# Optimization experiments

Measured on AMD Instinct MI355X. Metric: run time of the kernel, lower is better.

The kernel has to match this reference:

```python
import jax, jax.numpy as jnp
import numpy as np

N = 100000
E = 1600000
F_IN = 128
HID = 128
C = 10
NEG_SLOPE = 0.2


def setup_inputs() -> dict:
    key = jax.random.key(0)
    ks = jax.random.split(key, 12)
    x = jax.random.normal(ks[0], (N, F_IN), dtype=jnp.float32)
    edge_index = jax.random.randint(ks[1], (2, E), 0, N, dtype=jnp.int64)
    batch = jnp.zeros((N,), dtype=jnp.int64)
    s1 = 1.0 / np.sqrt(F_IN)
    s2 = 1.0 / np.sqrt(HID)
    return {
        "x": x,
        "edge_index": edge_index,
        "batch": batch,
        "W1": jax.random.normal(ks[2], (F_IN, HID), dtype=jnp.float32) * s1,
        "a_src1": jax.random.normal(ks[3], (HID,), dtype=jnp.float32) * s2,
        "a_dst1": jax.random.normal(ks[4], (HID,), dtype=jnp.float32) * s2,
        "b1": jnp.zeros((HID,), dtype=jnp.float32),
        "W2": jax.random.normal(ks[5], (HID, HID), dtype=jnp.float32) * s2,
        "a_src2": jax.random.normal(ks[6], (HID,), dtype=jnp.float32) * s2,
        "a_dst2": jax.random.normal(ks[7], (HID,), dtype=jnp.float32) * s2,
        "b2": jnp.zeros((HID,), dtype=jnp.float32),
        "Wlin": jax.random.normal(ks[8], (HID, C), dtype=jnp.float32) * s2,
        "blin": jnp.zeros((C,), dtype=jnp.float32),
    }


def gat_conv(x, src, dst, W, a_src, a_dst, b):
    # PyG GATConv, heads=1: h = xW; alpha_e = softmax_dst(leaky_relu(a_src.h[src] + a_dst.h[dst]))
    h = x @ W                                  # [N, H]
    alpha_s = h @ a_src                        # [N]
    alpha_d = h @ a_dst                        # [N]
    e = jax.nn.leaky_relu(alpha_s[src] + alpha_d[dst], NEG_SLOPE)  # [E]
    m = jax.ops.segment_max(e, dst, num_segments=N)                # per-dst max (stable softmax)
    ex = jnp.exp(e - m[dst])
    denom = jax.ops.segment_sum(ex, dst, num_segments=N)
    alpha = ex / (denom[dst] + 1e-16)          # [E]
    out = jax.ops.segment_sum(h[src] * alpha[:, None], dst, num_segments=N)
    return out + b


def reference(x, edge_index, batch, W1, a_src1, a_dst1, b1, W2, a_src2, a_dst2, b2, Wlin, blin):
    x = x.astype(jnp.float32)
    loops = jnp.arange(N, dtype=edge_index.dtype)
    src = jnp.concatenate([edge_index[0], loops])  # add_self_loops=True
    dst = jnp.concatenate([edge_index[1], loops])
    h = jax.nn.relu(gat_conv(x, src, dst, W1, a_src1, a_dst1, b1))
    h = jax.nn.relu(gat_conv(h, src, dst, W2, a_src2, a_dst2, b2))
    # dropout(p=0.5) is identity in eval mode
    return h @ Wlin + blin
```

## Files before the change

kernel.cpp:

```cpp
#include <hip/hip_runtime.h>

#define N_NODES 100000
#define N_EDGES 1600000
#define TOTE    (N_EDGES + N_NODES)
#define NEG     0.2f
#define NB      ((N_NODES + 255) >> 8)
#define BCAP    5120

typedef __attribute__((ext_vector_type(8))) short bf16x8;
typedef __attribute__((ext_vector_type(4))) float floatx4;

__device__ __forceinline__ unsigned short f2bf(float f) {
  unsigned int u = __float_as_uint(f);
  u += 0x7fffu + ((u >> 16) & 1u);
  return (unsigned short)(u >> 16);
}
__device__ __forceinline__ float bf_lo(unsigned int r) { return __uint_as_float(r << 16); }
__device__ __forceinline__ float bf_hi(unsigned int r) { return __uint_as_float(r & 0xffff0000u); }

__global__ __launch_bounds__(256) void k_wprep(const float* __restrict__ W1, const float* __restrict__ W2,
                                               unsigned short* __restrict__ B1hi, unsigned short* __restrict__ B1lo,
                                               unsigned short* __restrict__ B2hi, unsigned short* __restrict__ B2lo,
                                               int* __restrict__ bucketCnt) {
  int b = blockIdx.x;
  int t = threadIdx.x;
  if (b == 16) {
    for (int i = t; i < NB * 16; i += 256) bucketCnt[i] = 0;
    return;
  }
  const float* W = (b < 8) ? W1 : W2;
  unsigned short* Bh = (b < 8) ? B1hi : B2hi;
  unsigned short* Bl = (b < 8) ? B1lo : B2lo;
  int ntile = b & 7;
  int kq = t >> 6, lane = t & 63;
  int q = lane >> 4, m = lane & 15;
  int n = ntile * 16 + m;
  union { unsigned short us[8]; uint4 u4; } hi, lo;
#pragma unroll
  for (int j = 0; j < 8; ++j) {
    int k = kq * 32 + q * 8 + j;
    float w = W[(size_t)k * 128 + n];
    unsigned int u = __float_as_uint(w);
    hi.us[j] = (unsigned short)(u >> 16);
    float res = w - __uint_as_float(u & 0xffff0000u);
    lo.us[j] = f2bf(res);
  }
  size_t fo = ((size_t)(ntile * 4 + kq) * 64 + lane) * 8;
  *reinterpret_cast<uint4*>(Bh + fo) = hi.u4;
  *reinterpret_cast<uint4*>(Bl + fo) = lo.u4;
}

__global__ __launch_bounds__(256) void k_binA(const int* __restrict__ ei, int* __restrict__ bucketCnt,
                                              unsigned int* __restrict__ binned) {
  __shared__ int hist[NB];
  __shared__ int cur[NB];
  int t = threadIdx.x;
  for (int b = t; b < NB; b += 256) hist[b] = 0;
  __syncthreads();
  unsigned int pk[16]; int bk[16];
#pragma unroll
  for (int j = 0; j < 16; ++j) {
    int idx = blockIdx.x * 4096 + j * 256 + t;
    if (idx < N_EDGES) {
      int s = ei[idx], d = ei[N_EDGES + idx];
      bk[j] = d >> 8;
      pk[j] = ((unsigned int)s << 8) | (unsigned int)(d & 255);
      atomicAdd(&hist[bk[j]], 1);
    } else bk[j] = -1;
  }
  __syncthreads();
  for (int b = t; b < NB; b += 256) {
    int h = hist[b];
    if (h) cur[b] = b * BCAP + atomicAdd(&bucketCnt[b * 16], h);
  }
  __syncthreads();
#pragma unroll
  for (int j = 0; j < 16; ++j) {
    if (bk[j] >= 0) {
      int pos = atomicAdd(&cur[bk[j]], 1);
      binned[pos] = pk[j];
    }
  }
}

__global__ __launch_bounds__(512) void k_bin_scan(const int* __restrict__ bucketCnt,
                                                  int* __restrict__ binOffs) {
  __shared__ int sc[512];
  int t = threadIdx.x;
  int v = (t < NB) ? bucketCnt[t * 16] : 0;
  sc[t] = v; __syncthreads();
  for (int off = 1; off < 512; off <<= 1) {
    int x = (t >= off) ? sc[t - off] : 0;
    __syncthreads();
    sc[t] += x;
    __syncthreads();
  }
  int excl = sc[t] - v;
  if (t <= NB) binOffs[t] = excl;
}

__global__ __launch_bounds__(256) void k_binB(const unsigned int* __restrict__ binned,
                                              const int* __restrict__ binOffs,
                                              int* __restrict__ offs, int* __restrict__ srcs) {
  __shared__ int cnt[256];
  __shared__ int sc[256];
  __shared__ int cur[256];
  int b = blockIdx.x;
  int t = threadIdx.x;
  int node0 = b << 8;
  int nNodes = min(256, N_NODES - node0);
  int cntE = binOffs[b + 1] - binOffs[b];
  int e0 = b * BCAP, e1 = e0 + cntE;
  int base = binOffs[b] + node0;

  cnt[t] = 0; __syncthreads();
  for (int i = e0 + t; i < e1; i += 256) atomicAdd(&cnt[binned[i] & 255u], 1);
  __syncthreads();

  int v = (t < nNodes) ? cnt[t] + 1 : 0;
  sc[t] = v; __syncthreads();
  for (int off = 1; off < 256; off <<= 1) {
    int x = (t >= off) ? sc[t - off] : 0;
    __syncthreads();
    sc[t] += x;
    __syncthreads();
  }
  int excl = sc[t] - v;
  if (t < nNodes) {
    offs[node0 + t] = base + excl;
    srcs[base + excl] = node0 + t;
  }
  cur[t] = excl + 1;
  __syncthreads();

  for (int i = e0 + t; i < e1; i += 256) {
    unsigned int e = binned[i];
    int j = (int)(e & 255u);
    int s = (int)(e >> 8);
    int p = atomicAdd(&cur[j], 1);
    srcs[base + p] = s;
  }
  if (b == 0 && t == 0) offs[N_NODES] = TOTE;
}

template <bool SPLIT>
__global__ __launch_bounds__(256) void k_gemm_mfma(const void* __restrict__ Aptr,
                                                   const unsigned short* __restrict__ Bhi,
                                                   const unsigned short* __restrict__ Blo,
                                                   unsigned short* __restrict__ Cb,
                                                   const float* __restrict__ avS, const float* __restrict__ avD,
                                                   float* __restrict__ aS, float* __restrict__ aD,
                                                   float* __restrict__ slotS, float* __restrict__ slotD) {
  __shared__ unsigned short sC[64 * 136];
  __shared__ float redS[64 * 4], redD[64 * 4];
  __shared__ float mS[64], mD[64];
  int t = threadIdx.x;
  int w = t >> 6, lane = t & 63;
  int q = lane >> 4, m = lane & 15;
  int rbase = blockIdx.x * 64;

  floatx4 acc[4][2];
#pragma unroll
  for (int mt = 0; mt < 4; ++mt)
#pragma unroll
    for (int nt = 0; nt < 2; ++nt) acc[mt][nt] = (floatx4){0.f, 0.f, 0.f, 0.f};

#pragma unroll
  for (int k0 = 0; k0 < 4; ++k0) {
    bf16x8 Bh[2], Bl[2], Ah[4], Al[4];
#pragma unroll
    for (int nt = 0; nt < 2; ++nt) {
      int ntg = w * 2 + nt;
      size_t fo = ((size_t)(ntg * 4 + k0) * 64 + lane) * 8;
      Bh[nt] = *reinterpret_cast<const bf16x8*>(Bhi + fo);
      Bl[nt] = *reinterpret_cast<const bf16x8*>(Blo + fo);
    }
#pragma unroll
    for (int mt = 0; mt < 4; ++mt) {
      int row = rbase + mt * 16 + m;
      row = min(row, N_NODES - 1);
      if constexpr (SPLIT) {
        const float* ap = (const float*)Aptr + (size_t)row * 128 + k0 * 32 + q * 8;
        float4 v0 = *reinterpret_cast<const float4*>(ap);
        float4 v1 = *reinterpret_cast<const float4*>(ap + 4);
        float av[8] = {v0.x, v0.y, v0.z, v0.w, v1.x, v1.y, v1.z, v1.w};
        union { unsigned short us[8]; bf16x8 v; } uh, ul;
#pragma unroll
        for (int j = 0; j < 8; ++j) {
          unsigned int u = __float_as_uint(av[j]);
          uh.us[j] = (unsigned short)(u >> 16);
          float res = av[j] - __uint_as_float(u & 0xffff0000u);
          ul.us[j] = f2bf(res);
        }
        Ah[mt] = uh.v; Al[mt] = ul.v;
      } else {
        const unsigned short* ap = (const unsigned short*)Aptr + (size_t)row * 128 + k0 * 32 + q * 8;
        Ah[mt] = *reinterpret_cast<const bf16x8*>(ap);
      }
    }
#pragma unroll
    for (int mt = 0; mt < 4; ++mt)
#pragma unroll
      for (int nt = 0; nt < 2; ++nt) {
        acc[mt][nt] = __builtin_amdgcn_mfma_f32_16x16x32_bf16(Ah[mt], Bh[nt], acc[mt][nt], 0, 0, 0);
        acc[mt][nt] = __builtin_amdgcn_mfma_f32_16x16x32_bf16(Ah[mt], Bl[nt], acc[mt][nt], 0, 0, 0);
        if constexpr (SPLIT)
          acc[mt][nt] = __builtin_amdgcn_mfma_f32_16x16x32_bf16(Al[mt], Bh[nt], acc[mt][nt], 0, 0, 0);
      }
  }

  float avs[2], avd[2];
#pragma unroll
  for (int nt = 0; nt < 2; ++nt) {
    int c = w * 32 + nt * 16 + m;
    avs[nt] = avS[c];
    avd[nt] = avD[c];
  }
#pragma unroll
  for (int mt = 0; mt < 4; ++mt)
#pragma unroll
    for (int r = 0; r < 4; ++r) {
      float ps = acc[mt][0][r] * avs[0] + acc[mt][1][r] * avs[1];
      float pd = acc[mt][0][r] * avd[0] + acc[mt][1][r] * avd[1];
      ps += __shfl_xor(ps, 1); pd += __shfl_xor(pd, 1);
      ps += __shfl_xor(ps, 2); pd += __shfl_xor(pd, 2);
      ps += __shfl_xor(ps, 4); pd += __shfl_xor(pd, 4);
      ps += __shfl_xor(ps, 8); pd += __shfl_xor(pd, 8);
      if (m == 0) {
        int rl = mt * 16 + q * 4 + r;
        redS[rl * 4 + w] = ps;
        redD[rl * 4 + w] = pd;
      }
    }

#pragma unroll
  for (int mt = 0; mt < 4; ++mt)
#pragma unroll
    for (int nt = 0; nt < 2; ++nt)
#pragma unroll
      for (int r = 0; r < 4; ++r) {
        int rl = mt * 16 + q * 4 + r;
        int cl = w * 32 + nt * 16 + m;
        sC[rl * 136 + cl] = f2bf(acc[mt][nt][r]);
      }
  __syncthreads();

#pragma unroll
  for (int i = 0; i < 4; ++i) {
    int idx = i * 256 + t;
    int rl = idx >> 4, kk = idx & 15;
    int gr = rbase + rl;
    if (gr < N_NODES)
      *reinterpret_cast<uint4*>(Cb + (size_t)gr * 128 + kk * 8) =
          *reinterpret_cast<const uint4*>(sC + rl * 136 + kk * 8);
  }

  if (t < 64) {
    int gr = rbase + t;
    bool ok = gr < N_NODES;
    float ps = redS[t * 4] + redS[t * 4 + 1] + redS[t * 4 + 2] + redS[t * 4 + 3];
    float pd = redD[t * 4] + redD[t * 4 + 1] + redD[t * 4 + 2] + redD[t * 4 + 3];
    if (ok) { aS[gr] = ps; aD[gr] = pd; }
    mS[t] = ok ? ps : -1e30f;
    mD[t] = ok ? pd : -1e30f;
  }
  __syncthreads();
#pragma unroll
  for (int off = 32; off > 0; off >>= 1) {
    if (t < off) { mS[t] = fmaxf(mS[t], mS[t + off]); mD[t] = fmaxf(mD[t], mD[t + off]); }
    __syncthreads();
  }
  if (t == 0) { slotS[blockIdx.x] = mS[0]; slotD[blockIdx.x] = mD[0]; }
}

__global__ __launch_bounds__(256) void k_gmax(const float* __restrict__ slotS,
                                              const float* __restrict__ slotD,
                                              int n, float* __restrict__ gMh) {
  __shared__ float sS[256], sD[256];
  int t = threadIdx.x;
  float ms = -1e30f, md = -1e30f;
  for (int i = t; i < n; i += 256) { ms = fmaxf(ms, slotS[i]); md = fmaxf(md, slotD[i]); }
  sS[t] = ms; sD[t] = md;
  __syncthreads();
#pragma unroll
  for (int off = 128; off > 0; off >>= 1) {
    if (t < off) { sS[t] = fmaxf(sS[t], sS[t + off]); sD[t] = fmaxf(sD[t], sD[t + off]); }
    __syncthreads();
  }
  if (t == 0) {
    float M = sS[0] + sD[0];
    gMh[0] = (M > 0.f) ? M : NEG * M;
  }
}

#define FMA8(E, R)                                     \
  do {                                                 \
    acc[0] += (E) * bf_lo((R).x); acc[1] += (E) * bf_hi((R).x); \
    acc[2] += (E) * bf_lo((R).y); acc[3] += (E) * bf_hi((R).y); \
    acc[4] += (E) * bf_lo((R).z); acc[5] += (E) * bf_hi((R).z); \
    acc[6] += (E) * bf_lo((R).w); acc[7] += (E) * bf_hi((R).w); \
  } while (0)

__global__ __launch_bounds__(256) void k_aggregate(const unsigned short* __restrict__ hb,
                                                   const float* __restrict__ aS,
                                                   const float* __restrict__ aD,
                                                   const int* __restrict__ offs,
                                                   const int* __restrict__ srcs,
                                                   const float* __restrict__ bias,
                                                   const float* __restrict__ gMh,
                                                   unsigned short* __restrict__ outb) {
  __shared__ float2 pairs[16 * 17];
  int t = threadIdx.x;
  int g = t >> 4;
  int l = t & 15;
  int dst = blockIdx.x * 16 + g;
  float Mh = gMh[0];
  int beg = offs[dst], end = offs[dst + 1];
  float adn = aD[dst];
  float denom = 0.f;
  float acc[8];
#pragma unroll
  for (int k = 0; k < 8; ++k) acc[k] = 0.f;
  const int pbase = g * 17;

  for (int chunk = beg; chunk < end; chunk += 16) {
    int i = chunk + l;
    float ex = 0.f; int s = 0;
    if (i < end) {
      s = srcs[i];
      float e = aS[s] + adn;
      e = (e > 0.f) ? e : NEG * e;
      ex = __expf(e - Mh);
    }
    denom += ex;
    pairs[pbase + l] = make_float2(ex, __int_as_float(s));
    int cnt = min(16, end - chunk);
    int j = 0;
    for (; j + 4 <= cnt; j += 4) {
      float2 p0 = pairs[pbase + j + 0];
      float2 p1 = pairs[pbase + j + 1];
      float2 p2 = pairs[pbase + j + 2];
      float2 p3 = pairs[pbase + j + 3];
      uint4 r0 = *reinterpret_cast<const uint4*>(hb + (size_t)__float_as_int(p0.y) * 128 + l * 8);
      uint4 r1 = *reinterpret_cast<const uint4*>(hb + (size_t)__float_as_int(p1.y) * 128 + l * 8);
      uint4 r2 = *reinterpret_cast<const uint4*>(hb + (size_t)__float_as_int(p2.y) * 128 + l * 8);
      uint4 r3 = *reinterpret_cast<const uint4*>(hb + (size_t)__float_as_int(p3.y) * 128 + l * 8);
      FMA8(p0.x, r0);
      FMA8(p1.x, r1);
      FMA8(p2.x, r2);
      FMA8(p3.x, r3);
    }
    for (; j < cnt; ++j) {
      float2 pp = pairs[pbase + j];
      uint4 r = *reinterpret_cast<const uint4*>(hb + (size_t)__float_as_int(pp.y) * 128 + l * 8);
      FMA8(pp.x, r);
    }
  }
  denom += __shfl_xor(denom, 1);
  denom += __shfl_xor(denom, 2);
  denom += __shfl_xor(denom, 4);
  denom += __shfl_xor(denom, 8);
  float inv = 1.f / (denom + 1e-16f);
  float4 b0 = *reinterpret_cast<const float4*>(bias + l * 8);
  float4 b1 = *reinterpret_cast<const float4*>(bias + l * 8 + 4);
  float o0 = fmaxf(acc[0] * inv + b0.x, 0.f), o1 = fmaxf(acc[1] * inv + b0.y, 0.f);
  float o2 = fmaxf(acc[2] * inv + b0.z, 0.f), o3 = fmaxf(acc[3] * inv + b0.w, 0.f);
  float o4 = fmaxf(acc[4] * inv + b1.x, 0.f), o5 = fmaxf(acc[5] * inv + b1.y, 0.f);
  float o6 = fmaxf(acc[6] * inv + b1.z, 0.f), o7 = fmaxf(acc[7] * inv + b1.w, 0.f);
  union { unsigned short us[8]; uint4 u4; } oo;
  oo.us[0] = f2bf(o0); oo.us[1] = f2bf(o1); oo.us[2] = f2bf(o2); oo.us[3] = f2bf(o3);
  oo.us[4] = f2bf(o4); oo.us[5] = f2bf(o5); oo.us[6] = f2bf(o6); oo.us[7] = f2bf(o7);
  *reinterpret_cast<uint4*>(outb + (size_t)dst * 128 + l * 8) = oo.u4;
}

#define UNPK(V, B)                                     \
  do {                                                 \
    h[(B)+0] = bf_lo((V).x); h[(B)+1] = bf_hi((V).x);  \
    h[(B)+2] = bf_lo((V).y); h[(B)+3] = bf_hi((V).y);  \
    h[(B)+4] = bf_lo((V).z); h[(B)+5] = bf_hi((V).z);  \
    h[(B)+6] = bf_lo((V).w); h[(B)+7] = bf_hi((V).w);  \
  } while (0)

__global__ __launch_bounds__(256) void k_linear(const unsigned short* __restrict__ hb,
                                                const float* __restrict__ Wl,
                                                const float* __restrict__ bl,
                                                float* __restrict__ out) {
  __shared__ float sWt[10 * 144];
  __shared__ float sbl[10];
  int t = threadIdx.x;
  if (t < 128) {
    int jj = t >> 5, ii = t & 31;
#pragma unroll
    for (int c = 0; c < 10; ++c) sWt[c * 144 + jj * 36 + ii] = Wl[t * 10 + c];
  }
  if (t < 10) sbl[t] = bl[t];
  __syncthreads();
  int node = blockIdx.x * 64 + (t >> 2);
  int j = t & 3;
  if (node >= N_NODES) return;
  const unsigned short* hrow = hb + (size_t)node * 128 + j * 32;
  uint4 v0 = *reinterpret_cast<const uint4*>(hrow);
  uint4 v1 = *reinterpret_cast<const uint4*>(hrow + 8);
  uint4 v2 = *reinterpret_cast<const uint4*>(hrow + 16);
  uint4 v3 = *reinterpret_cast<const uint4*>(hrow + 24);
  float h[32];
  UNPK(v0, 0); UNPK(v1, 8); UNPK(v2, 16); UNPK(v3, 24);
  float p[10];
#pragma unroll
  for (int c = 0; c < 10; ++c) {
    const float4* wp = reinterpret_cast<const float4*>(&sWt[c * 144 + j * 36]);
    float s = 0.f;
#pragma unroll
    for (int qq = 0; qq < 8; ++qq) {
      float4 wv = wp[qq];
      s += h[qq * 4 + 0] * wv.x + h[qq * 4 + 1] * wv.y + h[qq * 4 + 2] * wv.z + h[qq * 4 + 3] * wv.w;
    }
    p[c] = s;
  }
#pragma unroll
  for (int c = 0; c < 10; ++c) {
    p[c] += __shfl_xor(p[c], 1);
    p[c] += __shfl_xor(p[c], 2);
  }
  if (j == 0) {
    float* orow = out + (size_t)node * 10;
    *reinterpret_cast<float2*>(orow + 0) = make_float2(p[0] + sbl[0], p[1] + sbl[1]);
    *reinterpret_cast<float2*>(orow + 2) = make_float2(p[2] + sbl[2], p[3] + sbl[3]);
    *reinterpret_cast<float2*>(orow + 4) = make_float2(p[4] + sbl[4], p[5] + sbl[5]);
    *reinterpret_cast<float2*>(orow + 6) = make_float2(p[6] + sbl[6], p[7] + sbl[7]);
    *reinterpret_cast<float2*>(orow + 8) = make_float2(p[8] + sbl[8], p[9] + sbl[9]);
  }
}

extern "C" void kernel_launch(void* const* d_in, const int* in_sizes, int n_in,
                              void* d_out, int out_size, void* d_ws, size_t ws_size,
                              hipStream_t stream) {
  const float* x   = (const float*)d_in[0];
  const int*   ei  = (const int*)d_in[1];
  const float* W1  = (const float*)d_in[3];
  const float* as1 = (const float*)d_in[4];
  const float* ad1 = (const float*)d_in[5];
  const float* b1  = (const float*)d_in[6];
  const float* W2  = (const float*)d_in[7];
  const float* as2 = (const float*)d_in[8];
  const float* ad2 = (const float*)d_in[9];
  const float* b2  = (const float*)d_in[10];
  const float* Wl  = (const float*)d_in[11];
  const float* bl  = (const float*)d_in[12];
  float* out = (float*)d_out;

  char* p = (char*)d_ws;
  unsigned short* hb   = (unsigned short*)p; p += (size_t)N_NODES * 128 * sizeof(unsigned short);
  unsigned short* hagg = (unsigned short*)p; p += (size_t)N_NODES * 128 * sizeof(unsigned short);
  float* aS    = (float*)p; p += (size_t)N_NODES * sizeof(float);
  float* aD    = (float*)p; p += (size_t)N_NODES * sizeof(float);
  int* offs    = (int*)p;   p += (size_t)(N_NODES + 4) * sizeof(int);
  int* srcs    = (int*)p;   p += (size_t)TOTE * sizeof(int);
  int* bucketCnt = (int*)p; p += (size_t)NB * 16 * sizeof(int);
  int* binOffs   = (int*)p; p += (size_t)(NB + 4) * sizeof(int);
  float* slotS = (float*)p; p += 2048 * sizeof(float);
  float* slotD = (float*)p; p += 2048 * sizeof(float);
  float* gMh = (float*)p;   p += 4 * sizeof(float);
  unsigned short* B1hi = (unsigned short*)p; p += 128 * 128 * sizeof(unsigned short);
  unsigned short* B1lo = (unsigned short*)p; p += 128 * 128 * sizeof(unsigned short);
  unsigned short* B2hi = (unsigned short*)p; p += 128 * 128 * sizeof(unsigned short);
  unsigned short* B2lo = (unsigned short*)p; p += 128 * 128 * sizeof(unsigned short);
  unsigned int* binned = (unsigned int*)hagg;

  int binBlocks = (N_EDGES + 4095) / 4096;

  k_wprep<<<17, 256, 0, stream>>>(W1, W2, B1hi, B1lo, B2hi, B2lo, bucketCnt);
  k_binA<<<binBlocks, 256, 0, stream>>>(ei, bucketCnt, binned);
  k_bin_scan<<<1, 512, 0, stream>>>(bucketCnt, binOffs);
  k_binB<<<NB, 256, 0, stream>>>(binned, binOffs, offs, srcs);

  int gemmBlocks = (N_NODES + 63) / 64;
  int aggBlocks  = N_NODES / 16;
  int linBlocks  = (N_NODES + 63) / 64;

  k_gemm_mfma<true><<<gemmBlocks, 256, 0, stream>>>(x, B1hi, B1lo, hb, as1, ad1, aS, aD, slotS, slotD);
  k_gmax<<<1, 256, 0, stream>>>(slotS, slotD, gemmBlocks, gMh);
  k_aggregate<<<aggBlocks, 256, 0, stream>>>(hb, aS, aD, offs, srcs, b1, gMh, hagg);
  k_gemm_mfma<false><<<gemmBlocks, 256, 0, stream>>>(hagg, B2hi, B2lo, hb, as2, ad2, aS, aD, slotS, slotD);
  k_gmax<<<1, 256, 0, stream>>>(slotS, slotD, gemmBlocks, gMh);
  k_aggregate<<<aggBlocks, 256, 0, stream>>>(hb, aS, aD, offs, srcs, b2, gMh, hagg);
  k_linear<<<linBlocks, 256, 0, stream>>>(hagg, Wl, bl, out);
}
```

Baseline: 365.3 us.

## Use one wavefront per destination with register-pipelined gathers; fuse final linear into aggregation

The aggregation kernel now assigns a full 64-lane wavefront to each destination node, with four 16-lane subgroups each handling a strided share of the edges. Edge weights and source indices are broadcast with shuffles instead of shared memory, and eight row gathers are kept in flight in registers. Partial sums are then reduced across subgroups. The second-layer aggregation also applies the final 128x10 linear layer directly, which removes the separate linear kernel and the round trip of the hidden features through memory. In exchange it uses more shuffles and more registers, and wastes lanes on low-degree nodes; it also shifts work per block from 16 to 4 destinations.

```diff
diff --git a/kernel.cpp b/kernel.cpp
--- a/kernel.cpp
+++ b/kernel.cpp
@@ -301,6 +301,7 @@
     acc[6] += (E) * bf_lo((R).w); acc[7] += (E) * bf_hi((R).w); \
   } while (0)
 
+template <bool FINAL>
 __global__ __launch_bounds__(256) void k_aggregate(const unsigned short* __restrict__ hb,
                                                    const float* __restrict__ aS,
                                                    const float* __restrict__ aD,
@@ -308,12 +309,27 @@
                                                    const int* __restrict__ srcs,
                                                    const float* __restrict__ bias,
                                                    const float* __restrict__ gMh,
-                                                   unsigned short* __restrict__ outb) {
-  __shared__ float2 pairs[16 * 17];
-  int t = threadIdx.x;
-  int g = t >> 4;
-  int l = t & 15;
-  int dst = blockIdx.x * 16 + g;
+                                                   unsigned short* __restrict__ outb,
+                                                   const float* __restrict__ Wl,
+                                                   const float* __restrict__ bl,
+                                                   float* __restrict__ out) {
+  __shared__ float sWt[10 * 144];
+  __shared__ float sbl[10];
+  int t = threadIdx.x;
+  if constexpr (FINAL) {
+    if (t < 128) {
+      int jj = t >> 5, ii = t & 31;
+#pragma unroll
+      for (int c = 0; c < 10; ++c) sWt[c * 144 + jj * 36 + ii] = Wl[t * 10 + c];
+    }
+    if (t < 10) sbl[t] = bl[t];
+    __syncthreads();
+  }
+  int w = t >> 6;
+  int tl = t & 63;
+  int sub = tl >> 4;
+  int l = tl & 15;
+  int dst = blockIdx.x * 4 + w;
   float Mh = gMh[0];
   int beg = offs[dst], end = offs[dst + 1];
   float adn = aD[dst];
@@ -321,114 +337,115 @@
   float acc[8];
 #pragma unroll
   for (int k = 0; k < 8; ++k) acc[k] = 0.f;
-  const int pbase = g * 17;
-
-  for (int chunk = beg; chunk < end; chunk += 16) {
-    int i = chunk + l;
-    float ex = 0.f; int s = 0;
+  const unsigned short* hbl = hb + l * 8;
+
+  uint4 r0, r1, r2, r3, r4, r5, r6, r7;
+
+  for (int base = beg; base < end; base += 64) {
+    int i = base + tl;
+    int sx = 0; float ex = 0.f;
     if (i < end) {
-      s = srcs[i];
-      float e = aS[s] + adn;
+      sx = srcs[i];
+      float e = aS[sx] + adn;
       e = (e > 0.f) ? e : NEG * e;
       ex = __expf(e - Mh);
     }
     denom += ex;
-    pairs[pbase + l] = make_float2(ex, __int_as_float(s));
-    int cnt = min(16, end - chunk);
-    int j = 0;
-    for (; j + 4 <= cnt; j += 4) {
-      float2 p0 = pairs[pbase + j + 0];
-      float2 p1 = pairs[pbase + j + 1];
-      float2 p2 = pairs[pbase + j + 2];
-      float2 p3 = pairs[pbase + j + 3];
-      uint4 r0 = *reinterpret_cast<const uint4*>(hb + (size_t)__float_as_int(p0.y) * 128 + l * 8);
-      uint4 r1 = *reinterpret_cast<const uint4*>(hb + (size_t)__float_as_int(p1.y) * 128 + l * 8);
-      uint4 r2 = *reinterpret_cast<const uint4*>(hb + (size_t)__float_as_int(p2.y) * 128 + l * 8);
-      uint4 r3 = *reinterpret_cast<const uint4*>(hb + (size_t)__float_as_int(p3.y) * 128 + l * 8);
-      FMA8(p0.x, r0);
-      FMA8(p1.x, r1);
-      FMA8(p2.x, r2);
-      FMA8(p3.x, r3);
-    }
-    for (; j < cnt; ++j) {
-      float2 pp = pairs[pbase + j];
-      uint4 r = *reinterpret_cast<const uint4*>(hb + (size_t)__float_as_int(pp.y) * 128 + l * 8);
-      FMA8(pp.x, r);
-    }
-  }
+    int cnt = end - base; if (cnt > 64) cnt = 64;
+
+#define BS(P) __shfl(sx, 4 * (P) + sub, 64)
+#define BE(P) __shfl(ex, 4 * (P) + sub, 64)
+#define ISS(R, P)                                                                   \
+    do {                                                                            \
+      if (4 * (P) < cnt) {                                                          \
+        int s_ = BS(P);                                                             \
+        R = *reinterpret_cast<const uint4*>(hbl + ((size_t)(unsigned)s_ << 7));     \
+      }                                                                             \
+    } while (0)
+#define STP(R, P)                       \
+    do {                                \
+      float e_ = BE(P);                 \
+      FMA8(e_, R);                      \
+      ISS(R, (P) + 8);                  \
+    } while (0)
+
+    ISS(r0, 0); ISS(r1, 1); ISS(r2, 2); ISS(r3, 3);
+    ISS(r4, 4); ISS(r5, 5); ISS(r6, 6); ISS(r7, 7);
+    do {
+      STP(r0, 0);  if (cnt <= 4)  break;
+      STP(r1, 1);  if (cnt <= 8)  break;
+      STP(r2, 2);  if (cnt <= 12) break;
+      STP(r3, 3);  if (cnt <= 16) break;
+      STP(r4, 4);  if (cnt <= 20) break;
+      STP(r5, 5);  if (cnt <= 24) break;
+      STP(r6, 6);  if (cnt <= 28) break;
+      STP(r7, 7);  if (cnt <= 32) break;
+      STP(r0, 8);  if (cnt <= 36) break;
+      STP(r1, 9);  if (cnt <= 40) break;
+      STP(r2, 10); if (cnt <= 44) break;
+      STP(r3, 11); if (cnt <= 48) break;
+      STP(r4, 12); if (cnt <= 52) break;
+      STP(r5, 13); if (cnt <= 56) break;
+      STP(r6, 14); if (cnt <= 60) break;
+      STP(r7, 15);
+    } while (0);
+#undef BS
+#undef BE
+#undef ISS
+#undef STP
+  }
+
   denom += __shfl_xor(denom, 1);
   denom += __shfl_xor(denom, 2);
   denom += __shfl_xor(denom, 4);
   denom += __shfl_xor(denom, 8);
+  denom += __shfl_xor(denom, 16);
+  denom += __shfl_xor(denom, 32);
   float inv = 1.f / (denom + 1e-16f);
+#pragma unroll
+  for (int k = 0; k < 8; ++k) {
+    acc[k] += __shfl_xor(acc[k], 16);
+    acc[k] += __shfl_xor(acc[k], 32);
+  }
+
   float4 b0 = *reinterpret_cast<const float4*>(bias + l * 8);
   float4 b1 = *reinterpret_cast<const float4*>(bias + l * 8 + 4);
   float o0 = fmaxf(acc[0] * inv + b0.x, 0.f), o1 = fmaxf(acc[1] * inv + b0.y, 0.f);
   float o2 = fmaxf(acc[2] * inv + b0.z, 0.f), o3 = fmaxf(acc[3] * inv + b0.w, 0.f);
   float o4 = fmaxf(acc[4] * inv + b1.x, 0.f), o5 = fmaxf(acc[5] * inv + b1.y, 0.f);
   float o6 = fmaxf(acc[6] * inv + b1.z, 0.f), o7 = fmaxf(acc[7] * inv + b1.w, 0.f);
-  union { unsigned short us[8]; uint4 u4; } oo;
-  oo.us[0] = f2bf(o0); oo.us[1] = f2bf(o1); oo.us[2] = f2bf(o2); oo.us[3] = f2bf(o3);
-  oo.us[4] = f2bf(o4); oo.us[5] = f2bf(o5); oo.us[6] = f2bf(o6); oo.us[7] = f2bf(o7);
-  *reinterpret_cast<uint4*>(outb + (size_t)dst * 128 + l * 8) = oo.u4;
-}
-
-#define UNPK(V, B)                                     \
-  do {                                                 \
-    h[(B)+0] = bf_lo((V).x); h[(B)+1] = bf_hi((V).x);  \
-    h[(B)+2] = bf_lo((V).y); h[(B)+3] = bf_hi((V).y);  \
-    h[(B)+4] = bf_lo((V).z); h[(B)+5] = bf_hi((V).z);  \
-    h[(B)+6] = bf_lo((V).w); h[(B)+7] = bf_hi((V).w);  \
-  } while (0)
-
-__global__ __launch_bounds__(256) void k_linear(const unsigned short* __restrict__ hb,
-                                                const float* __restrict__ Wl,
-                                                const float* __restrict__ bl,
-                                                float* __restrict__ out) {
-  __shared__ float sWt[10 * 144];
-  __shared__ float sbl[10];
-  int t = threadIdx.x;
-  if (t < 128) {
-    int jj = t >> 5, ii = t & 31;
-#pragma unroll
-    for (int c = 0; c < 10; ++c) sWt[c * 144 + jj * 36 + ii] = Wl[t * 10 + c];
-  }
-  if (t < 10) sbl[t] = bl[t];
-  __syncthreads();
-  int node = blockIdx.x * 64 + (t >> 2);
-  int j = t & 3;
-  if (node >= N_NODES) return;
-  const unsigned short* hrow = hb + (size_t)node * 128 + j * 32;
-  uint4 v0 = *reinterpret_cast<const uint4*>(hrow);
-  uint4 v1 = *reinterpret_cast<const uint4*>(hrow + 8);
-  uint4 v2 = *reinterpret_cast<const uint4*>(hrow + 16);
-  uint4 v3 = *reinterpret_cast<const uint4*>(hrow + 24);
-  float h[32];
-  UNPK(v0, 0); UNPK(v1, 8); UNPK(v2, 16); UNPK(v3, 24);
-  float p[10];
-#pragma unroll
-  for (int c = 0; c < 10; ++c) {
-    const float4* wp = reinterpret_cast<const float4*>(&sWt[c * 144 + j * 36]);
-    float s = 0.f;
-#pragma unroll
-    for (int qq = 0; qq < 8; ++qq) {
-      float4 wv = wp[qq];
-      s += h[qq * 4 + 0] * wv.x + h[qq * 4 + 1] * wv.y + h[qq * 4 + 2] * wv.z + h[qq * 4 + 3] * wv.w;
-    }
-    p[c] = s;
-  }
-#pragma unroll
-  for (int c = 0; c < 10; ++c) {
-    p[c] += __shfl_xor(p[c], 1);
-    p[c] += __shfl_xor(p[c], 2);
-  }
-  if (j == 0) {
-    float* orow = out + (size_t)node * 10;
-    *reinterpret_cast<float2*>(orow + 0) = make_float2(p[0] + sbl[0], p[1] + sbl[1]);
-    *reinterpret_cast<float2*>(orow + 2) = make_float2(p[2] + sbl[2], p[3] + sbl[3]);
-    *reinterpret_cast<float2*>(orow + 4) = make_float2(p[4] + sbl[4], p[5] + sbl[5]);
-    *reinterpret_cast<float2*>(orow + 6) = make_float2(p[6] + sbl[6], p[7] + sbl[7]);
-    *reinterpret_cast<float2*>(orow + 8) = make_float2(p[8] + sbl[8], p[9] + sbl[9]);
+
+  if constexpr (!FINAL) {
+    if (sub == 0) {
+      union { unsigned short us[8]; uint4 u4; } oo;
+      oo.us[0] = f2bf(o0); oo.us[1] = f2bf(o1); oo.us[2] = f2bf(o2); oo.us[3] = f2bf(o3);
+      oo.us[4] = f2bf(o4); oo.us[5] = f2bf(o5); oo.us[6] = f2bf(o6); oo.us[7] = f2bf(o7);
+      *reinterpret_cast<uint4*>(outb + (size_t)dst * 128 + l * 8) = oo.u4;
+    }
+  } else {
+    float p[10];
+#pragma unroll
+    for (int c = 0; c < 10; ++c) {
+      const float4* wp = reinterpret_cast<const float4*>(&sWt[c * 144 + (l >> 2) * 36 + (l & 3) * 8]);
+      float4 w0 = wp[0], w1 = wp[1];
+      p[c] = o0 * w0.x + o1 * w0.y + o2 * w0.z + o3 * w0.w +
+             o4 * w1.x + o5 * w1.y + o6 * w1.z + o7 * w1.w;
+    }
+#pragma unroll
+    for (int c = 0; c < 10; ++c) {
+      p[c] += __shfl_xor(p[c], 1);
+      p[c] += __shfl_xor(p[c], 2);
+      p[c] += __shfl_xor(p[c], 4);
+      p[c] += __shfl_xor(p[c], 8);
+    }
+    if (tl == 0) {
+      float* orow = out + (size_t)dst * 10;
+      *reinterpret_cast<float2*>(orow + 0) = make_float2(p[0] + sbl[0], p[1] + sbl[1]);
+      *reinterpret_cast<float2*>(orow + 2) = make_float2(p[2] + sbl[2], p[3] + sbl[3]);
+      *reinterpret_cast<float2*>(orow + 4) = make_float2(p[4] + sbl[4], p[5] + sbl[5]);
+      *reinterpret_cast<float2*>(orow + 6) = make_float2(p[6] + sbl[6], p[7] + sbl[7]);
+      *reinterpret_cast<float2*>(orow + 8) = make_float2(p[8] + sbl[8], p[9] + sbl[9]);
+    }
   }
 }
 
@@ -475,14 +492,14 @@
   k_binB<<<NB, 256, 0, stream>>>(binned, binOffs, offs, srcs);
 
   int gemmBlocks = (N_NODES + 63) / 64;
-  int aggBlocks  = N_NODES / 16;
-  int linBlocks  = (N_NODES + 63) / 64;
+  int aggBlocks  = N_NODES / 4;
 
   k_gemm_mfma<true><<<gemmBlocks, 256, 0, stream>>>(x, B1hi, B1lo, hb, as1, ad1, aS, aD, slotS, slotD);
   k_gmax<<<1, 256, 0, stream>>>(slotS, slotD, gemmBlocks, gMh);
-  k_aggregate<<<aggBlocks, 256, 0, stream>>>(hb, aS, aD, offs, srcs, b1, gMh, hagg);
+  k_aggregate<false><<<aggBlocks, 256, 0, stream>>>(hb, aS, aD, offs, srcs, b1, gMh, hagg,
+                                                    nullptr, nullptr, nullptr);
   k_gemm_mfma<false><<<gemmBlocks, 256, 0, stream>>>(hagg, B2hi, B2lo, hb, as2, ad2, aS, aD, slotS, slotD);
   k_gmax<<<1, 256, 0, stream>>>(slotS, slotD, gemmBlocks, gMh);
-  k_aggregate<<<aggBlocks, 256, 0, stream>>>(hb, aS, aD, offs, srcs, b2, gMh, hagg);
-  k_linear<<<linBlocks, 256, 0, stream>>>(hagg, Wl, bl, out);
-}
+  k_aggregate<true><<<aggBlocks, 256, 0, stream>>>(hb, aS, aD, offs, srcs, b2, gMh, hagg,
+                                                   Wl, bl, out);
+}
```

Result: slower. 421.5 us (+15.4%).

## Fuse final linear into second aggregation and double-buffer neighbor gathers

Applied to the files above, without the earlier changes.

The second GAT aggregation now computes the 128x10 output projection directly from its registers and uses a 16-lane shuffle reduction. This removes the separate linear kernel, the bf16 write and re-read of the hidden layer, and one launch. The aggregation inner loop is also software-pipelined: it alternates two register sets so the next four neighbor-row gathers are issued before the current four are accumulated. Short groups still load four rows, padding with zero-weight loads of row 0, which adds a few wasted cached reads per chunk. The fused variant also uses more shared memory per block.

```diff
diff --git a/kernel.cpp b/kernel.cpp
--- a/kernel.cpp
+++ b/kernel.cpp
@@ -301,6 +301,22 @@
     acc[6] += (E) * bf_lo((R).w); acc[7] += (E) * bf_hi((R).w); \
   } while (0)
 
+#define LDG(R0, R1, R2, R3, E0, E1, E2, E3, J)                                                   \
+  do {                                                                                           \
+    float2 q0 = pairs[pbase + (J) + 0];                                                          \
+    float2 q1 = pairs[pbase + (J) + 1];                                                          \
+    float2 q2 = pairs[pbase + (J) + 2];                                                          \
+    float2 q3 = pairs[pbase + (J) + 3];                                                          \
+    E0 = q0.x; E1 = q1.x; E2 = q2.x; E3 = q3.x;                                                  \
+    R0 = *reinterpret_cast<const uint4*>(hbl + ((size_t)(unsigned)__float_as_int(q0.y) << 7));   \
+    R1 = *reinterpret_cast<const uint4*>(hbl + ((size_t)(unsigned)__float_as_int(q1.y) << 7));   \
+    R2 = *reinterpret_cast<const uint4*>(hbl + ((size_t)(unsigned)__float_as_int(q2.y) << 7));   \
+    R3 = *reinterpret_cast<const uint4*>(hbl + ((size_t)(unsigned)__float_as_int(q3.y) << 7));   \
+  } while (0)
+#define FMAG(R0, R1, R2, R3, E0, E1, E2, E3) \
+  do { FMA8(E0, R0); FMA8(E1, R1); FMA8(E2, R2); FMA8(E3, R3); } while (0)
+
+template <bool FINAL>
 __global__ __launch_bounds__(256) void k_aggregate(const unsigned short* __restrict__ hb,
                                                    const float* __restrict__ aS,
                                                    const float* __restrict__ aD,
@@ -308,9 +324,23 @@
                                                    const int* __restrict__ srcs,
                                                    const float* __restrict__ bias,
                                                    const float* __restrict__ gMh,
-                                                   unsigned short* __restrict__ outb) {
+                                                   unsigned short* __restrict__ outb,
+                                                   const float* __restrict__ Wl,
+                                                   const float* __restrict__ bl,
+                                                   float* __restrict__ out) {
   __shared__ float2 pairs[16 * 17];
-  int t = threadIdx.x;
+  __shared__ float sWt[FINAL ? 10 * 144 : 1];
+  __shared__ float sbl[FINAL ? 16 : 1];
+  int t = threadIdx.x;
+  if constexpr (FINAL) {
+    if (t < 128) {
+      int jj = t >> 5, ii = t & 31;
+#pragma unroll
+      for (int c = 0; c < 10; ++c) sWt[c * 144 + jj * 36 + ii] = Wl[t * 10 + c];
+    }
+    if (t < 10) sbl[t] = bl[t];
+    __syncthreads();
+  }
   int g = t >> 4;
   int l = t & 15;
   int dst = blockIdx.x * 16 + g;
@@ -322,6 +352,10 @@
 #pragma unroll
   for (int k = 0; k < 8; ++k) acc[k] = 0.f;
   const int pbase = g * 17;
+  const unsigned short* hbl = hb + l * 8;
+
+  uint4 ra0, ra1, ra2, ra3, rb0, rb1, rb2, rb3;
+  float ea0, ea1, ea2, ea3, eb0, eb1, eb2, eb3;
 
   for (int chunk = beg; chunk < end; chunk += 16) {
     int i = chunk + l;
@@ -334,28 +368,23 @@
     }
     denom += ex;
     pairs[pbase + l] = make_float2(ex, __int_as_float(s));
-    int cnt = min(16, end - chunk);
+    int cnt = end - chunk; if (cnt > 16) cnt = 16;
+    LDG(ra0, ra1, ra2, ra3, ea0, ea1, ea2, ea3, 0);
     int j = 0;
-    for (; j + 4 <= cnt; j += 4) {
-      float2 p0 = pairs[pbase + j + 0];
-      float2 p1 = pairs[pbase + j + 1];
-      float2 p2 = pairs[pbase + j + 2];
-      float2 p3 = pairs[pbase + j + 3];
-      uint4 r0 = *reinterpret_cast<const uint4*>(hb + (size_t)__float_as_int(p0.y) * 128 + l * 8);
-      uint4 r1 = *reinterpret_cast<const uint4*>(hb + (size_t)__float_as_int(p1.y) * 128 + l * 8);
-      uint4 r2 = *reinterpret_cast<const uint4*>(hb + (size_t)__float_as_int(p2.y) * 128 + l * 8);
-      uint4 r3 = *reinterpret_cast<const uint4*>(hb + (size_t)__float_as_int(p3.y) * 128 + l * 8);
-      FMA8(p0.x, r0);
-      FMA8(p1.x, r1);
-      FMA8(p2.x, r2);
-      FMA8(p3.x, r3);
-    }
-    for (; j < cnt; ++j) {
-      float2 pp = pairs[pbase + j];
-      uint4 r = *reinterpret_cast<const uint4*>(hb + (size_t)__float_as_int(pp.y) * 128 + l * 8);
-      FMA8(pp.x, r);
-    }
-  }
+    for (;;) {
+      bool more = (j + 4) < cnt;
+      if (more) LDG(rb0, rb1, rb2, rb3, eb0, eb1, eb2, eb3, j + 4);
+      FMAG(ra0, ra1, ra2, ra3, ea0, ea1, ea2, ea3);
+      j += 4;
+      if (!more) break;
+      bool more2 = (j + 4) < cnt;
+      if (more2) LDG(ra0, ra1, ra2, ra3, ea0, ea1, ea2, ea3, j + 4);
+      FMAG(rb0, rb1, rb2, rb3, eb0, eb1, eb2, eb3);
+      j += 4;
+      if (!more2) break;
+    }
+  }
+
   denom += __shfl_xor(denom, 1);
   denom += __shfl_xor(denom, 2);
   denom += __shfl_xor(denom, 4);
@@ -367,68 +396,36 @@
   float o2 = fmaxf(acc[2] * inv + b0.z, 0.f), o3 = fmaxf(acc[3] * inv + b0.w, 0.f);
   float o4 = fmaxf(acc[4] * inv + b1.x, 0.f), o5 = fmaxf(acc[5] * inv + b1.y, 0.f);
   float o6 = fmaxf(acc[6] * inv + b1.z, 0.f), o7 = fmaxf(acc[7] * inv + b1.w, 0.f);
-  union { unsigned short us[8]; uint4 u4; } oo;
-  oo.us[0] = f2bf(o0); oo.us[1] = f2bf(o1); oo.us[2] = f2bf(o2); oo.us[3] = f2bf(o3);
-  oo.us[4] = f2bf(o4); oo.us[5] = f2bf(o5); oo.us[6] = f2bf(o6); oo.us[7] = f2bf(o7);
-  *reinterpret_cast<uint4*>(outb + (size_t)dst * 128 + l * 8) = oo.u4;
-}
-
-#define UNPK(V, B)                                     \
-  do {                                                 \
-    h[(B)+0] = bf_lo((V).x); h[(B)+1] = bf_hi((V).x);  \
-    h[(B)+2] = bf_lo((V).y); h[(B)+3] = bf_hi((V).y);  \
-    h[(B)+4] = bf_lo((V).z); h[(B)+5] = bf_hi((V).z);  \
-    h[(B)+6] = bf_lo((V).w); h[(B)+7] = bf_hi((V).w);  \
-  } while (0)
-
-__global__ __launch_bounds__(256) void k_linear(const unsigned short* __restrict__ hb,
-                                                const float* __restrict__ Wl,
-                                                const float* __restrict__ bl,
-                                                float* __restrict__ out) {
-  __shared__ float sWt[10 * 144];
-  __shared__ float sbl[10];
-  int t = threadIdx.x;
-  if (t < 128) {
-    int jj = t >> 5, ii = t & 31;
-#pragma unroll
-    for (int c = 0; c < 10; ++c) sWt[c * 144 + jj * 36 + ii] = Wl[t * 10 + c];
-  }
-  if (t < 10) sbl[t] = bl[t];
-  __syncthreads();
-  int node = blockIdx.x * 64 + (t >> 2);
-  int j = t & 3;
-  if (node >= N_NODES) return;
-  const unsigned short* hrow = hb + (size_t)node * 128 + j * 32;
-  uint4 v0 = *reinterpret_cast<const uint4*>(hrow);
-  uint4 v1 = *reinterpret_cast<const uint4*>(hrow + 8);
-  uint4 v2 = *reinterpret_cast<const uint4*>(hrow + 16);
-  uint4 v3 = *reinterpret_cast<const uint4*>(hrow + 24);
-  float h[32];
-  UNPK(v0, 0); UNPK(v1, 8); UNPK(v2, 16); UNPK(v3, 24);
-  float p[10];
-#pragma unroll
-  for (int c = 0; c < 10; ++c) {
-    const float4* wp = reinterpret_cast<const float4*>(&sWt[c * 144 + j * 36]);
-    float s = 0.f;
-#pragma unroll
-    for (int qq = 0; qq < 8; ++qq) {
-      float4 wv = wp[qq];
-      s += h[qq * 4 + 0] * wv.x + h[qq * 4 + 1] * wv.y + h[qq * 4 + 2] * wv.z + h[qq * 4 + 3] * wv.w;
-    }
-    p[c] = s;
-  }
-#pragma unroll
-  for (int c = 0; c < 10; ++c) {
-    p[c] += __shfl_xor(p[c], 1);
-    p[c] += __shfl_xor(p[c], 2);
-  }
-  if (j == 0) {
-    float* orow = out + (size_t)node * 10;
-    *reinterpret_cast<float2*>(orow + 0) = make_float2(p[0] + sbl[0], p[1] + sbl[1]);
-    *reinterpret_cast<float2*>(orow + 2) = make_float2(p[2] + sbl[2], p[3] + sbl[3]);
-    *reinterpret_cast<float2*>(orow + 4) = make_float2(p[4] + sbl[4], p[5] + sbl[5]);
-    *reinterpret_cast<float2*>(orow + 6) = make_float2(p[6] + sbl[6], p[7] + sbl[7]);
-    *reinterpret_cast<float2*>(orow + 8) = make_float2(p[8] + sbl[8], p[9] + sbl[9]);
+
+  if constexpr (!FINAL) {
+    union { unsigned short us[8]; uint4 u4; } oo;
+    oo.us[0] = f2bf(o0); oo.us[1] = f2bf(o1); oo.us[2] = f2bf(o2); oo.us[3] = f2bf(o3);
+    oo.us[4] = f2bf(o4); oo.us[5] = f2bf(o5); oo.us[6] = f2bf(o6); oo.us[7] = f2bf(o7);
+    *reinterpret_cast<uint4*>(outb + (size_t)dst * 128 + l * 8) = oo.u4;
+  } else {
+    float p[10];
+#pragma unroll
+    for (int c = 0; c < 10; ++c) {
+      const float4* wp = reinterpret_cast<const float4*>(&sWt[c * 144 + (l >> 2) * 36 + (l & 3) * 8]);
+      float4 w0 = wp[0], w1 = wp[1];
+      p[c] = o0 * w0.x + o1 * w0.y + o2 * w0.z + o3 * w0.w +
+             o4 * w1.x + o5 * w1.y + o6 * w1.z + o7 * w1.w;
+    }
+#pragma unroll
+    for (int c = 0; c < 10; ++c) {
+      p[c] += __shfl_xor(p[c], 1);
+      p[c] += __shfl_xor(p[c], 2);
+      p[c] += __shfl_xor(p[c], 4);
+      p[c] += __shfl_xor(p[c], 8);
+    }
+    if (l == 0) {
+      float* orow = out + (size_t)dst * 10;
+      *reinterpret_cast<float2*>(orow + 0) = make_float2(p[0] + sbl[0], p[1] + sbl[1]);
+      *reinterpret_cast<float2*>(orow + 2) = make_float2(p[2] + sbl[2], p[3] + sbl[3]);
+      *reinterpret_cast<float2*>(orow + 4) = make_float2(p[4] + sbl[4], p[5] + sbl[5]);
+      *reinterpret_cast<float2*>(orow + 6) = make_float2(p[6] + sbl[6], p[7] + sbl[7]);
+      *reinterpret_cast<float2*>(orow + 8) = make_float2(p[8] + sbl[8], p[9] + sbl[9]);
+    }
   }
 }
 
@@ -476,13 +473,13 @@
 
   int gemmBlocks = (N_NODES + 63) / 64;
   int aggBlocks  = N_NODES / 16;
-  int linBlocks  = (N_NODES + 63) / 64;
 
   k_gemm_mfma<true><<<gemmBlocks, 256, 0, stream>>>(x, B1hi, B1lo, hb, as1, ad1, aS, aD, slotS, slotD);
   k_gmax<<<1, 256, 0, stream>>>(slotS, slotD, gemmBlocks, gMh);
-  k_aggregate<<<aggBlocks, 256, 0, stream>>>(hb, aS, aD, offs, srcs, b1, gMh, hagg);
+  k_aggregate<false><<<aggBlocks, 256, 0, stream>>>(hb, aS, aD, offs, srcs, b1, gMh, hagg,
+                                                    nullptr, nullptr, nullptr);
   k_gemm_mfma<false><<<gemmBlocks, 256, 0, stream>>>(hagg, B2hi, B2lo, hb, as2, ad2, aS, aD, slotS, slotD);
   k_gmax<<<1, 256, 0, stream>>>(slotS, slotD, gemmBlocks, gMh);
-  k_aggregate<<<aggBlocks, 256, 0, stream>>>(hb, aS, aD, offs, srcs, b2, gMh, hagg);
-  k_linear<<<linBlocks, 256, 0, stream>>>(hagg, Wl, bl, out);
-}
+  k_aggregate<true><<<aggBlocks, 256, 0, stream>>>(hb, aS, aD, offs, srcs, b2, gMh, hagg,
+                                                   Wl, bl, out);
+}
```

Result: faster. 353.1 us (-3.3%).
